# Performance work log

Measured on AMD Instinct MI355X. Metric: run time of the kernel, lower is better.

The kernel has to match this reference:

```python
import jax, jax.numpy as jnp
import numpy as np

N_NODES = 50000
N_EDGES = 800000
IN_CH = 64
HID = 64
EDGE_DIM = 16


def _glorot(key, shape):
    fan_in, fan_out = shape[0], shape[1]
    lim = (6.0 / (fan_in + fan_out)) ** 0.5
    return jax.random.uniform(key, shape, jnp.float32, -lim, lim)


def setup_inputs() -> dict:
    key = jax.random.key(0)
    ks = jax.random.split(key, 12)
    x = jax.random.normal(ks[0], (N_NODES, IN_CH), jnp.float32)
    edge_index = jax.random.randint(ks[1], (2, N_EDGES), 0, N_NODES, jnp.int64)
    edge_attr = jax.random.normal(ks[2], (N_EDGES, EDGE_DIM), jnp.float32)
    # SAGEConv1: lin_l (aggregated neighbors, with bias) + lin_r (root, no bias)
    W1l = _glorot(ks[3], (IN_CH, HID)); b1l = jnp.zeros((HID,), jnp.float32)
    W1r = _glorot(ks[4], (IN_CH, HID))
    # SAGEConv2
    W2l = _glorot(ks[5], (HID, HID)); b2l = jnp.zeros((HID,), jnp.float32)
    W2r = _glorot(ks[6], (HID, HID))
    # edge MLP: Linear(2*HID+EDGE_DIM -> HID), ReLU, Linear(HID -> 1)
    Wm1 = _glorot(ks[7], (2 * HID + EDGE_DIM, HID))
    bm1 = jnp.zeros((HID,), jnp.float32)
    Wm2 = _glorot(ks[8], (HID, 1))
    bm2 = jnp.zeros((1,), jnp.float32)
    return dict(x=x, edge_index=edge_index, edge_attr=edge_attr,
                W1l=W1l, b1l=b1l, W1r=W1r,
                W2l=W2l, b2l=b2l, W2r=W2r,
                Wm1=Wm1, bm1=bm1, Wm2=Wm2, bm2=bm2)


def _sage_conv(x, src, dst, deg_inv, Wl, bl, Wr):
    # mean aggregation of source-node features at destination nodes
    n = x.shape[0]
    agg = jax.ops.segment_sum(x[src], dst, num_segments=n)  # [N, d]
    agg = agg * deg_inv  # mean over incoming edges
    return agg @ Wl + bl + x @ Wr


def reference(x, edge_index, edge_attr, W1l, b1l, W1r, W2l, b2l, W2r, Wm1, bm1, Wm2, bm2):
    src, dst = edge_index[0], edge_index[1]
    n = x.shape[0]
    # in-degree (over dst), clamped to 1 as in PyG mean aggregation
    deg = jax.ops.segment_sum(jnp.ones((src.shape[0],), x.dtype), dst, num_segments=n)
    deg_inv = (1.0 / jnp.maximum(deg, 1.0))[:, None]  # [N,1]

    h = jax.nn.relu(_sage_conv(x, src, dst, deg_inv, W1l, b1l, W1r))
    h = jax.nn.relu(_sage_conv(h, src, dst, deg_inv, W2l, b2l, W2r))

    # gather endpoint embeddings + concat with edge features -> MLP score
    edge_input = jnp.concatenate([h[src], h[dst], edge_attr], axis=-1)  # [E, 2H+De]
    hidden = jax.nn.relu(edge_input @ Wm1 + bm1)
    return (hidden @ Wm2 + bm2).squeeze(-1)  # [E]
```

## Files before the change

### kernel.cpp

```cpp
#include <hip/hip_runtime.h>
#include <hip/hip_bf16.h>


#define C 64
#define KP 168
#define SK 136
#define TILE_E 64
#define WSHIFT 12

typedef short short8 __attribute__((ext_vector_type(8)));
typedef float f32x4 __attribute__((ext_vector_type(4)));

__device__ __forceinline__ unsigned short f2bf(float f) {
    unsigned int u = __float_as_uint(f);
    return (unsigned short)((u + 0x7FFFu + ((u >> 16) & 1u)) >> 16);
}
__device__ __forceinline__ unsigned int pack2(float lo, float hi) {
    return (unsigned int)f2bf(lo) | ((unsigned int)f2bf(hi) << 16);
}
__device__ __forceinline__ float bflo(unsigned int u) { return __uint_as_float(u << 16); }
__device__ __forceinline__ float bfhi(unsigned int u) { return __uint_as_float(u & 0xFFFF0000u); }

__global__ void prep(const int* __restrict__ dst, int* __restrict__ degi,
                     const float* __restrict__ ea, unsigned short* __restrict__ eaB,
                     const float* __restrict__ x, unsigned short* __restrict__ xB,
                     int E, int nx8, int doEa) {
    int i = blockIdx.x * blockDim.x + threadIdx.x;
    if (i < E) atomicAdd(&degi[dst[i]], 1);
    if (doEa && i < 2 * E) {
        const float4* p = (const float4*)(ea + (size_t)i * 8);
        float4 a = p[0], b = p[1];
        uint4 o;
        o.x = pack2(a.x, a.y); o.y = pack2(a.z, a.w);
        o.z = pack2(b.x, b.y); o.w = pack2(b.z, b.w);
        *(uint4*)(eaB + (size_t)i * 8) = o;
    }
    if (i < nx8) {
        const float4* p = (const float4*)(x + (size_t)i * 8);
        float4 a = p[0], b = p[1];
        uint4 o;
        o.x = pack2(a.x, a.y); o.y = pack2(a.z, a.w);
        o.z = pack2(b.x, b.y); o.w = pack2(b.z, b.w);
        *(uint4*)(xB + (size_t)i * 8) = o;
    }
}

__global__ __launch_bounds__(256) void scan_partial(const int* __restrict__ degi,
        int* __restrict__ rowptr, int* __restrict__ partials, int N) {
    __shared__ int sWs[4];
    int t = threadIdx.x, b = blockIdx.x;
    int g0 = b * 1024 + t * 4;
    int v0 = (g0 + 0 < N) ? degi[g0 + 0] : 0;
    int v1 = (g0 + 1 < N) ? degi[g0 + 1] : 0;
    int v2 = (g0 + 2 < N) ? degi[g0 + 2] : 0;
    int v3 = (g0 + 3 < N) ? degi[g0 + 3] : 0;
    int tsum = v0 + v1 + v2 + v3;
    int lane = t & 63, w = t >> 6;
    int incl = tsum;
    #pragma unroll
    for (int m = 1; m < 64; m <<= 1) {
        int y = __shfl_up(incl, m, 64);
        if (lane >= m) incl += y;
    }
    if (lane == 63) sWs[w] = incl;
    __syncthreads();
    int wprefix = 0;
    for (int i = 0; i < w; ++i) wprefix += sWs[i];
    int run = wprefix + incl - tsum;
    if (g0 + 0 < N) rowptr[g0 + 0] = run; run += v0;
    if (g0 + 1 < N) rowptr[g0 + 1] = run; run += v1;
    if (g0 + 2 < N) rowptr[g0 + 2] = run; run += v2;
    if (g0 + 3 < N) rowptr[g0 + 3] = run;
    if (t == 255) partials[b] = wprefix + incl;
}

__global__ __launch_bounds__(256) void scan_add_fused(int* __restrict__ rowptr,
        const int* __restrict__ partials, int* __restrict__ cursor,
        const int* __restrict__ degi, float* __restrict__ deg_inv,
        int N, int E, int nb) {
    __shared__ int sOff[64];
    int t = threadIdx.x;
    if (t < 64) {
        int v = (t < nb) ? partials[t] : 0;
        int incl = v;
        #pragma unroll
        for (int m = 1; m < 64; m <<= 1) {
            int y = __shfl_up(incl, m, 64);
            if (t >= m) incl += y;
        }
        sOff[t] = incl - v;
    }
    __syncthreads();
    int i = blockIdx.x * 256 + t;
    if (i < N) {
        int r = rowptr[i] + sOff[i >> 10];
        rowptr[i] = r;
        cursor[i] = r;
        deg_inv[i] = 1.0f / fmaxf((float)degi[i], 1.0f);
    }
    if (i == 0) rowptr[N] = E;
}

__global__ __launch_bounds__(256) void fill_csr_xcd(const int* __restrict__ src,
        const int* __restrict__ dst, int* __restrict__ cursor,
        int* __restrict__ eSrc, int E) {
    int g = blockIdx.x & 7;
    int tid = (blockIdx.x >> 3) * 256 + threadIdx.x;
    int stride = (gridDim.x >> 3) * 256;
    for (int e = tid; e < E; e += stride) {
        int d = dst[e];
        if (((d >> WSHIFT) & 7) == g) {
            int pos = atomicAdd(&cursor[d], 1);
            eSrc[pos] = src[e];
        }
    }
}

__global__ __launch_bounds__(256) void csr_agg_bf16(const unsigned short* __restrict__ fB,
        const int* __restrict__ rowptr, const int* __restrict__ eSrc,
        const float* __restrict__ deg_inv, unsigned short* __restrict__ aggB, int N) {
    int node = blockIdx.x * 4 + (threadIdx.x >> 6);
    if (node >= N) return;
    int lane = threadIdx.x & 63;
    int s8 = lane >> 3, ci = lane & 7;
    int row = rowptr[node], end = rowptr[node + 1];
    float a[8] = {0.f, 0.f, 0.f, 0.f, 0.f, 0.f, 0.f, 0.f};
    int j = row;
    for (; j + 16 <= end; j += 16) {
        int sA = eSrc[j + s8];
        int sB = eSrc[j + 8 + s8];
        uint4 vA = *(const uint4*)(fB + (size_t)sA * C + ci * 8);
        uint4 vB = *(const uint4*)(fB + (size_t)sB * C + ci * 8);
        a[0] += bflo(vA.x); a[1] += bfhi(vA.x);
        a[2] += bflo(vA.y); a[3] += bfhi(vA.y);
        a[4] += bflo(vA.z); a[5] += bfhi(vA.z);
        a[6] += bflo(vA.w); a[7] += bfhi(vA.w);
        a[0] += bflo(vB.x); a[1] += bfhi(vB.x);
        a[2] += bflo(vB.y); a[3] += bfhi(vB.y);
        a[4] += bflo(vB.z); a[5] += bfhi(vB.z);
        a[6] += bflo(vB.w); a[7] += bfhi(vB.w);
    }
    for (; j < end; j += 8) {
        if (j + s8 < end) {
            int s = eSrc[j + s8];
            uint4 v = *(const uint4*)(fB + (size_t)s * C + ci * 8);
            a[0] += bflo(v.x); a[1] += bfhi(v.x);
            a[2] += bflo(v.y); a[3] += bfhi(v.y);
            a[4] += bflo(v.z); a[5] += bfhi(v.z);
            a[6] += bflo(v.w); a[7] += bfhi(v.w);
        }
    }
    #pragma unroll
    for (int m = 8; m < 64; m <<= 1)
        #pragma unroll
        for (int k = 0; k < 8; ++k)
            a[k] += __shfl_xor(a[k], m, 64);
    if (s8 == 0) {
        float di = deg_inv[node];
        uint4 o;
        o.x = pack2(a[0] * di, a[1] * di);
        o.y = pack2(a[2] * di, a[3] * di);
        o.z = pack2(a[4] * di, a[5] * di);
        o.w = pack2(a[6] * di, a[7] * di);
        *(uint4*)(aggB + (size_t)node * C + ci * 8) = o;
    }
}

__global__ __launch_bounds__(256) void dense_mfma(
        const unsigned short* __restrict__ aB, const unsigned short* __restrict__ xB,
        const float* __restrict__ Wl, const float* __restrict__ Wr,
        const float* __restrict__ bl, unsigned short* __restrict__ hOut, int N) {
    __shared__ unsigned short sW[C * SK];
    __shared__ unsigned short sAB[C * SK];
    int t = threadIdx.x;
    int lane = t & 63, w = t >> 6;
    int l15 = lane & 15, quad = lane >> 4;
    int n0 = blockIdx.x * 64;

    for (int i = t; i < 128 * C; i += 256) {
        int k = i >> 6, n = i & 63;
        float v = (k < C) ? Wl[k * C + n] : Wr[(k - C) * C + n];
        sW[n * SK + k] = f2bf(v);
    }
    for (int i = t; i < 64 * 16; i += 256) {
        int r = i >> 4, ch = i & 15;
        int node = n0 + r;
        uint4 v = {0u, 0u, 0u, 0u};
        if (node < N)
            v = (ch < 8) ? *(const uint4*)(aB + (size_t)node * C + ch * 8)
                         : *(const uint4*)(xB + (size_t)node * C + (ch - 8) * 8);
        *(uint4*)&sAB[r * SK + ch * 8] = v;
    }
    __syncthreads();

    short8 bW[4][4];
    #pragma unroll
    for (int t4 = 0; t4 < 4; ++t4)
        #pragma unroll
        for (int kc = 0; kc < 4; ++kc)
            bW[t4][kc] = *(const short8*)&sW[(t4 * 16 + l15) * SK + kc * 32 + quad * 8];
    float blr[4];
    #pragma unroll
    for (int t4 = 0; t4 < 4; ++t4) blr[t4] = bl[t4 * 16 + l15];

    f32x4 acc[4] = {{0.f, 0.f, 0.f, 0.f}, {0.f, 0.f, 0.f, 0.f},
                    {0.f, 0.f, 0.f, 0.f}, {0.f, 0.f, 0.f, 0.f}};
    #pragma unroll
    for (int kc = 0; kc < 4; ++kc) {
        short8 a = *(const short8*)&sAB[(w * 16 + l15) * SK + kc * 32 + quad * 8];
        #pragma unroll
        for (int t4 = 0; t4 < 4; ++t4)
            acc[t4] = __builtin_amdgcn_mfma_f32_16x16x32_bf16(a, bW[t4][kc], acc[t4], 0, 0, 0);
    }
    __syncthreads();

    #pragma unroll
    for (int t4 = 0; t4 < 4; ++t4)
        #pragma unroll
        for (int r = 0; r < 4; ++r) {
            int rl = w * 16 + quad * 4 + r;
            sW[rl * 72 + t4 * 16 + l15] = f2bf(fmaxf(acc[t4][r] + blr[t4], 0.f));
        }
    __syncthreads();
    for (int i = t; i < 64 * 8; i += 256) {
        int r = i >> 3, c8 = i & 7;
        int node = n0 + r;
        if (node < N)
            *(uint4*)(hOut + (size_t)node * C + c8 * 8) = *(const uint4*)&sW[r * 72 + c8 * 8];
    }
}

template <bool EAB>
__device__ __forceinline__ void gather_rows(const unsigned short* __restrict__ hB,
        const unsigned short* __restrict__ eaB, const float* __restrict__ ea,
        int s, int d, int idxc, int quad,
        uint4& u0, uint4& u1, uint4& u2, uint4& u3, uint4& u4) {
    const uint4* ps = (const uint4*)(hB + (size_t)s * C);
    const uint4* pd = (const uint4*)(hB + (size_t)d * C);
    u0 = ps[quad];
    u1 = ps[4 + quad];
    u2 = pd[quad];
    u3 = pd[4 + quad];
    u4.x = 0u; u4.y = 0u; u4.z = 0u; u4.w = 0u;
    if (quad < 2) {
        if (EAB) {
            u4 = *(const uint4*)(eaB + (size_t)idxc * 16 + quad * 8);
        } else {
            const float4* pe = (const float4*)(ea + (size_t)idxc * 16 + quad * 8);
            float4 f0 = pe[0], f1 = pe[1];
            u4.x = pack2(f0.x, f0.y); u4.y = pack2(f0.z, f0.w);
            u4.z = pack2(f1.x, f1.y); u4.w = pack2(f1.z, f1.w);
        }
    }
}

template <bool EAB>
__global__ __launch_bounds__(256) void edge_mlp_pipe(
        const unsigned short* __restrict__ hB, const int* __restrict__ src,
        const int* __restrict__ dst, const float* __restrict__ ea,
        const unsigned short* __restrict__ eaB,
        const float* __restrict__ Wm1, const float* __restrict__ bm1,
        const float* __restrict__ Wm2, const float* __restrict__ bm2,
        float* __restrict__ out, int E, int nTiles) {
    __shared__ unsigned short sW[C * KP];
    int t = threadIdx.x;
    int lane = t & 63, w = t >> 6;
    int l15 = lane & 15, quad = lane >> 4;

    for (int i = t; i < C * 3; i += 256) {
        int r = i / 3, cc = 144 + (i % 3) * 8;
        uint4 z = {0u, 0u, 0u, 0u};
        *(uint4*)&sW[r * KP + cc] = z;
    }
    for (int i = t; i < 144 * C; i += 256) {
        int k = i >> 6, n = i & 63;
        sW[n * KP + k] = f2bf(Wm1[i]);
    }
    __syncthreads();

    short8 bW[4][5];
    #pragma unroll
    for (int t4 = 0; t4 < 4; ++t4)
        #pragma unroll
        for (int kc = 0; kc < 5; ++kc)
            bW[t4][kc] = *(const short8*)&sW[(t4 * 16 + l15) * KP + kc * 32 + quad * 8];
    float bmr[4], w2r[4];
    #pragma unroll
    for (int t4 = 0; t4 < 4; ++t4) {
        int j = t4 * 16 + l15;
        bmr[t4] = bm1[j];
        w2r[t4] = Wm2[j];
    }
    float bb = bm2[0];

    int stride = gridDim.x;
    int lbase = w * 16 + l15;

    int tile = blockIdx.x;
    int idxc = min(tile * TILE_E + lbase, E - 1);
    int s = src[idxc], d = dst[idxc];
    int tileN = tile + stride;
    int idxNc = (tileN < nTiles) ? min(tileN * TILE_E + lbase, E - 1) : idxc;
    int sN = src[idxNc], dN = dst[idxNc];
    uint4 cu0, cu1, cu2, cu3, cu4;
    gather_rows<EAB>(hB, eaB, ea, s, d, idxc, quad, cu0, cu1, cu2, cu3, cu4);

    while (true) {
        bool hasNext = (tileN < nTiles);
        uint4 nu0, nu1, nu2, nu3, nu4;
        gather_rows<EAB>(hB, eaB, ea, sN, dN, idxNc, quad, nu0, nu1, nu2, nu3, nu4);
        int tileNN = tileN + stride;
        int idxNNc = (tileNN < nTiles) ? min(tileNN * TILE_E + lbase, E - 1) : idxNc;
        int sNN = src[idxNNc], dNN = dst[idxNNc];

        short8 a0 = *(short8*)&cu0, a1 = *(short8*)&cu1, a2 = *(short8*)&cu2,
               a3 = *(short8*)&cu3, a4 = *(short8*)&cu4;
        f32x4 acc[4] = {{0.f, 0.f, 0.f, 0.f}, {0.f, 0.f, 0.f, 0.f},
                        {0.f, 0.f, 0.f, 0.f}, {0.f, 0.f, 0.f, 0.f}};
        #pragma unroll
        for (int t4 = 0; t4 < 4; ++t4) {
            acc[t4] = __builtin_amdgcn_mfma_f32_16x16x32_bf16(a0, bW[t4][0], acc[t4], 0, 0, 0);
            acc[t4] = __builtin_amdgcn_mfma_f32_16x16x32_bf16(a1, bW[t4][1], acc[t4], 0, 0, 0);
            acc[t4] = __builtin_amdgcn_mfma_f32_16x16x32_bf16(a2, bW[t4][2], acc[t4], 0, 0, 0);
            acc[t4] = __builtin_amdgcn_mfma_f32_16x16x32_bf16(a3, bW[t4][3], acc[t4], 0, 0, 0);
            acc[t4] = __builtin_amdgcn_mfma_f32_16x16x32_bf16(a4, bW[t4][4], acc[t4], 0, 0, 0);
        }

        float sres[4];
        #pragma unroll
        for (int r = 0; r < 4; ++r) {
            float v = 0.f;
            #pragma unroll
            for (int t4 = 0; t4 < 4; ++t4)
                v += fmaxf(acc[t4][r] + bmr[t4], 0.f) * w2r[t4];
            #pragma unroll
            for (int m = 1; m < 16; m <<= 1)
                v += __shfl_xor(v, m, 16);
            sres[r] = v;
        }
        if (l15 == 0) {
            int e0 = tile * TILE_E;
            #pragma unroll
            for (int r = 0; r < 4; ++r) {
                int e = e0 + w * 16 + quad * 4 + r;
                if (e < E) out[e] = sres[r] + bb;
            }
        }

        if (!hasNext) break;
        tile = tileN; tileN = tileNN;
        idxc = idxNc; idxNc = idxNNc;
        s = sN; sN = sNN; d = dN; dN = dNN;
        cu0 = nu0; cu1 = nu1; cu2 = nu2; cu3 = nu3; cu4 = nu4;
    }
}

extern "C" void kernel_launch(void* const* d_in, const int* in_sizes, int n_in,
                              void* d_out, int out_size, void* d_ws, size_t ws_size,
                              hipStream_t stream) {
    const float* x   = (const float*)d_in[0];
    const int*   ei  = (const int*)d_in[1];
    const float* ea  = (const float*)d_in[2];
    const float* W1l = (const float*)d_in[3];
    const float* b1l = (const float*)d_in[4];
    const float* W1r = (const float*)d_in[5];
    const float* W2l = (const float*)d_in[6];
    const float* b2l = (const float*)d_in[7];
    const float* W2r = (const float*)d_in[8];
    const float* Wm1 = (const float*)d_in[9];
    const float* bm1 = (const float*)d_in[10];
    const float* Wm2 = (const float*)d_in[11];
    const float* bm2 = (const float*)d_in[12];
    float* out = (float*)d_out;

    const int N = in_sizes[0] / C;
    const int E = in_sizes[1] / 2;
    const int* src = ei;
    const int* dst = ei + E;

    char* wsb = (char*)d_ws;
    int npad = (N + 1023) & ~1023;
    float* deg_inv = (float*)wsb;                wsb += (size_t)npad * 4;
    unsigned short* xB   = (unsigned short*)wsb; wsb += (size_t)npad * C * 2;
    unsigned short* h1B  = (unsigned short*)wsb; wsb += (size_t)npad * C * 2;
    unsigned short* h2B  = (unsigned short*)wsb; wsb += (size_t)npad * C * 2;
    unsigned short* aggB = (unsigned short*)wsb; wsb += (size_t)npad * C * 2;
    int* degi    = (int*)wsb;                    wsb += (size_t)npad * 4;
    int* rowptr  = (int*)wsb;                    wsb += (size_t)(npad + 64) * 4;
    int* cursor  = (int*)wsb;                    wsb += (size_t)npad * 4;
    int* eSrc    = (int*)wsb;                    wsb += (size_t)E * 4;
    int* partials = (int*)wsb;                   wsb += 64 * 4;
    unsigned short* eaB = (unsigned short*)wsb;
    size_t used = (size_t)(wsb - (char*)d_ws);
    int useEaB = (ws_size >= used + (size_t)E * 16 * 2) ? 1 : 0;

    int tpb = 256;
    int nb = (N + 1023) / 1024;
    int nx8 = N * C / 8;

    hipMemsetAsync(degi, 0, (size_t)N * sizeof(int), stream);
    int prepN = (2 * E > nx8) ? 2 * E : nx8;
    prep<<<(prepN + tpb - 1) / tpb, tpb, 0, stream>>>(dst, degi, ea, eaB, x, xB, E, nx8, useEaB);
    scan_partial<<<nb, tpb, 0, stream>>>(degi, rowptr, partials, N);
    scan_add_fused<<<(N + tpb - 1) / tpb, tpb, 0, stream>>>(rowptr, partials, cursor,
            degi, deg_inv, N, E, nb);
    fill_csr_xcd<<<1024, tpb, 0, stream>>>(src, dst, cursor, eSrc, E);

    csr_agg_bf16<<<(N + 3) / 4, tpb, 0, stream>>>(xB, rowptr, eSrc, deg_inv, aggB, N);
    dense_mfma<<<(N + 63) / 64, tpb, 0, stream>>>(aggB, xB, W1l, W1r, b1l, h1B, N);

    csr_agg_bf16<<<(N + 3) / 4, tpb, 0, stream>>>(h1B, rowptr, eSrc, deg_inv, aggB, N);
    dense_mfma<<<(N + 63) / 64, tpb, 0, stream>>>(aggB, h1B, W2l, W2r, b2l, h2B, N);

    int nTiles = (E + TILE_E - 1) / TILE_E;
    int grid = nTiles < 2048 ? nTiles : 2048;
    if (useEaB)
        edge_mlp_pipe<true><<<grid, tpb, 0, stream>>>(h2B, src, dst, ea, eaB,
                Wm1, bm1, Wm2, bm2, out, E, nTiles);
    else
        edge_mlp_pipe<false><<<grid, tpb, 0, stream>>>(h2B, src, dst, ea, eaB,
                Wm1, bm1, Wm2, bm2, out, E, nTiles);
}
```

Measured before the change: 303.2 us.

## Split CSR aggregation across channel halves per XCD and drop edge_attr bf16 precast

The CSR mean-aggregation kernel now gives each node's two 32-channel halves to different blocks. The low block-id bits select the channel half, so blocks that share an XCD read the same half of the feature table, which is meant to raise L2 locality. Each wave now covers 16 edges per iteration with 4 lanes per edge instead of 8. Separately, the prep kernel no longer converts edge_attr to bf16, and the edge MLP converts the fp32 edge features inline instead. This removes a full extra pass over edge_attr, in exchange for double the edge-feature bytes read in the edge kernel and twice as many eSrc index loads during aggregation.

After: 338.9 us. +11.7%, slower.

```diff
diff --git a/kernel.cpp b/kernel.cpp
--- a/kernel.cpp
+++ b/kernel.cpp
@@ -22,19 +22,10 @@
 __device__ __forceinline__ float bfhi(unsigned int u) { return __uint_as_float(u & 0xFFFF0000u); }
 
 __global__ void prep(const int* __restrict__ dst, int* __restrict__ degi,
-                     const float* __restrict__ ea, unsigned short* __restrict__ eaB,
                      const float* __restrict__ x, unsigned short* __restrict__ xB,
-                     int E, int nx8, int doEa) {
+                     int E, int nx8) {
     int i = blockIdx.x * blockDim.x + threadIdx.x;
     if (i < E) atomicAdd(&degi[dst[i]], 1);
-    if (doEa && i < 2 * E) {
-        const float4* p = (const float4*)(ea + (size_t)i * 8);
-        float4 a = p[0], b = p[1];
-        uint4 o;
-        o.x = pack2(a.x, a.y); o.y = pack2(a.z, a.w);
-        o.z = pack2(b.x, b.y); o.w = pack2(b.z, b.w);
-        *(uint4*)(eaB + (size_t)i * 8) = o;
-    }
     if (i < nx8) {
         const float4* p = (const float4*)(x + (size_t)i * 8);
         float4 a = p[0], b = p[1];
@@ -116,34 +107,23 @@
     }
 }
 
-__global__ __launch_bounds__(256) void csr_agg_bf16(const unsigned short* __restrict__ fB,
+__global__ __launch_bounds__(256) void csr_agg_half(const unsigned short* __restrict__ fB,
         const int* __restrict__ rowptr, const int* __restrict__ eSrc,
         const float* __restrict__ deg_inv, unsigned short* __restrict__ aggB, int N) {
-    int node = blockIdx.x * 4 + (threadIdx.x >> 6);
+    int b = blockIdx.x;
+    int g = b & 7;
+    int node = (b >> 3) * 16 + (g & 3) * 4 + (threadIdx.x >> 6);
     if (node >= N) return;
     int lane = threadIdx.x & 63;
-    int s8 = lane >> 3, ci = lane & 7;
+    int slot = lane >> 2, cg = lane & 3;
+    int choff = (g >> 2) * 32 + cg * 8;
     int row = rowptr[node], end = rowptr[node + 1];
     float a[8] = {0.f, 0.f, 0.f, 0.f, 0.f, 0.f, 0.f, 0.f};
-    int j = row;
-    for (; j + 16 <= end; j += 16) {
-        int sA = eSrc[j + s8];
-        int sB = eSrc[j + 8 + s8];
-        uint4 vA = *(const uint4*)(fB + (size_t)sA * C + ci * 8);
-        uint4 vB = *(const uint4*)(fB + (size_t)sB * C + ci * 8);
-        a[0] += bflo(vA.x); a[1] += bfhi(vA.x);
-        a[2] += bflo(vA.y); a[3] += bfhi(vA.y);
-        a[4] += bflo(vA.z); a[5] += bfhi(vA.z);
-        a[6] += bflo(vA.w); a[7] += bfhi(vA.w);
-        a[0] += bflo(vB.x); a[1] += bfhi(vB.x);
-        a[2] += bflo(vB.y); a[3] += bfhi(vB.y);
-        a[4] += bflo(vB.z); a[5] += bfhi(vB.z);
-        a[6] += bflo(vB.w); a[7] += bfhi(vB.w);
-    }
-    for (; j < end; j += 8) {
-        if (j + s8 < end) {
-            int s = eSrc[j + s8];
-            uint4 v = *(const uint4*)(fB + (size_t)s * C + ci * 8);
+    for (int j0 = row; j0 < end; j0 += 16) {
+        int j = j0 + slot;
+        if (j < end) {
+            int s = eSrc[j];
+            uint4 v = *(const uint4*)(fB + (size_t)s * C + choff);
             a[0] += bflo(v.x); a[1] += bfhi(v.x);
             a[2] += bflo(v.y); a[3] += bfhi(v.y);
             a[4] += bflo(v.z); a[5] += bfhi(v.z);
@@ -151,18 +131,18 @@
         }
     }
     #pragma unroll
-    for (int m = 8; m < 64; m <<= 1)
+    for (int m = 4; m < 64; m <<= 1)
         #pragma unroll
         for (int k = 0; k < 8; ++k)
             a[k] += __shfl_xor(a[k], m, 64);
-    if (s8 == 0) {
+    if (slot == 0) {
         float di = deg_inv[node];
         uint4 o;
         o.x = pack2(a[0] * di, a[1] * di);
         o.y = pack2(a[2] * di, a[3] * di);
         o.z = pack2(a[4] * di, a[5] * di);
         o.w = pack2(a[6] * di, a[7] * di);
-        *(uint4*)(aggB + (size_t)node * C + ci * 8) = o;
+        *(uint4*)(aggB + (size_t)node * C + choff) = o;
     }
 }
 
@@ -230,10 +210,8 @@
     }
 }
 
-template <bool EAB>
 __device__ __forceinline__ void gather_rows(const unsigned short* __restrict__ hB,
-        const unsigned short* __restrict__ eaB, const float* __restrict__ ea,
-        int s, int d, int idxc, int quad,
+        const float* __restrict__ ea, int s, int d, int idxc, int quad,
         uint4& u0, uint4& u1, uint4& u2, uint4& u3, uint4& u4) {
     const uint4* ps = (const uint4*)(hB + (size_t)s * C);
     const uint4* pd = (const uint4*)(hB + (size_t)d * C);
@@ -243,22 +221,16 @@
     u3 = pd[4 + quad];
     u4.x = 0u; u4.y = 0u; u4.z = 0u; u4.w = 0u;
     if (quad < 2) {
-        if (EAB) {
-            u4 = *(const uint4*)(eaB + (size_t)idxc * 16 + quad * 8);
-        } else {
-            const float4* pe = (const float4*)(ea + (size_t)idxc * 16 + quad * 8);
-            float4 f0 = pe[0], f1 = pe[1];
-            u4.x = pack2(f0.x, f0.y); u4.y = pack2(f0.z, f0.w);
-            u4.z = pack2(f1.x, f1.y); u4.w = pack2(f1.z, f1.w);
-        }
-    }
-}
-
-template <bool EAB>
+        const float4* pe = (const float4*)(ea + (size_t)idxc * 16 + quad * 8);
+        float4 f0 = pe[0], f1 = pe[1];
+        u4.x = pack2(f0.x, f0.y); u4.y = pack2(f0.z, f0.w);
+        u4.z = pack2(f1.x, f1.y); u4.w = pack2(f1.z, f1.w);
+    }
+}
+
 __global__ __launch_bounds__(256) void edge_mlp_pipe(
         const unsigned short* __restrict__ hB, const int* __restrict__ src,
         const int* __restrict__ dst, const float* __restrict__ ea,
-        const unsigned short* __restrict__ eaB,
         const float* __restrict__ Wm1, const float* __restrict__ bm1,
         const float* __restrict__ Wm2, const float* __restrict__ bm2,
         float* __restrict__ out, int E, int nTiles) {
@@ -303,12 +275,12 @@
     int idxNc = (tileN < nTiles) ? min(tileN * TILE_E + lbase, E - 1) : idxc;
     int sN = src[idxNc], dN = dst[idxNc];
     uint4 cu0, cu1, cu2, cu3, cu4;
-    gather_rows<EAB>(hB, eaB, ea, s, d, idxc, quad, cu0, cu1, cu2, cu3, cu4);
+    gather_rows(hB, ea, s, d, idxc, quad, cu0, cu1, cu2, cu3, cu4);
 
     while (true) {
         bool hasNext = (tileN < nTiles);
         uint4 nu0, nu1, nu2, nu3, nu4;
-        gather_rows<EAB>(hB, eaB, ea, sN, dN, idxNc, quad, nu0, nu1, nu2, nu3, nu4);
+        gather_rows(hB, ea, sN, dN, idxNc, quad, nu0, nu1, nu2, nu3, nu4);
         int tileNN = tileN + stride;
         int idxNNc = (tileNN < nTiles) ? min(tileNN * TILE_E + lbase, E - 1) : idxNc;
         int sNN = src[idxNNc], dNN = dst[idxNNc];
@@ -390,34 +362,28 @@
     int* cursor  = (int*)wsb;                    wsb += (size_t)npad * 4;
     int* eSrc    = (int*)wsb;                    wsb += (size_t)E * 4;
     int* partials = (int*)wsb;                   wsb += 64 * 4;
-    unsigned short* eaB = (unsigned short*)wsb;
-    size_t used = (size_t)(wsb - (char*)d_ws);
-    int useEaB = (ws_size >= used + (size_t)E * 16 * 2) ? 1 : 0;
 
     int tpb = 256;
     int nb = (N + 1023) / 1024;
     int nx8 = N * C / 8;
 
     hipMemsetAsync(degi, 0, (size_t)N * sizeof(int), stream);
-    int prepN = (2 * E > nx8) ? 2 * E : nx8;
-    prep<<<(prepN + tpb - 1) / tpb, tpb, 0, stream>>>(dst, degi, ea, eaB, x, xB, E, nx8, useEaB);
+    int prepN = (E > nx8) ? E : nx8;
+    prep<<<(prepN + tpb - 1) / tpb, tpb, 0, stream>>>(dst, degi, x, xB, E, nx8);
     scan_partial<<<nb, tpb, 0, stream>>>(degi, rowptr, partials, N);
     scan_add_fused<<<(N + tpb - 1) / tpb, tpb, 0, stream>>>(rowptr, partials, cursor,
             degi, deg_inv, N, E, nb);
     fill_csr_xcd<<<1024, tpb, 0, stream>>>(src, dst, cursor, eSrc, E);
 
-    csr_agg_bf16<<<(N + 3) / 4, tpb, 0, stream>>>(xB, rowptr, eSrc, deg_inv, aggB, N);
+    int aggGrid = 8 * ((N + 15) / 16);
+    csr_agg_half<<<aggGrid, tpb, 0, stream>>>(xB, rowptr, eSrc, deg_inv, aggB, N);
     dense_mfma<<<(N + 63) / 64, tpb, 0, stream>>>(aggB, xB, W1l, W1r, b1l, h1B, N);
 
-    csr_agg_bf16<<<(N + 3) / 4, tpb, 0, stream>>>(h1B, rowptr, eSrc, deg_inv, aggB, N);
+    csr_agg_half<<<aggGrid, tpb, 0, stream>>>(h1B, rowptr, eSrc, deg_inv, aggB, N);
     dense_mfma<<<(N + 63) / 64, tpb, 0, stream>>>(aggB, h1B, W2l, W2r, b2l, h2B, N);
 
     int nTiles = (E + TILE_E - 1) / TILE_E;
     int grid = nTiles < 2048 ? nTiles : 2048;
-    if (useEaB)
-        edge_mlp_pipe<true><<<grid, tpb, 0, stream>>>(h2B, src, dst, ea, eaB,
-                Wm1, bm1, Wm2, bm2, out, E, nTiles);
-    else
-        edge_mlp_pipe<false><<<grid, tpb, 0, stream>>>(h2B, src, dst, ea, eaB,
-                Wm1, bm1, Wm2, bm2, out, E, nTiles);
-}
+    edge_mlp_pipe<<<grid, tpb, 0, stream>>>(h2B, src, dst, ea,
+            Wm1, bm1, Wm2, bm2, out, E, nTiles);
+}
```
